# Optimization experiments

Hardware: AMD Instinct MI355X
Metric: run time of the kernel (lower is better)

The kernel has to match this reference:

```python
import jax, jax.numpy as jnp
import numpy as np

D = 1152      # model dim
E = 4         # num_experts
HID = 768     # llama FFN hidden: multiple_of*ceil(int(2*1152/3)/256)
NH = 8        # cross-attention heads
TEMP = 2.0    # expert gumbel temperature (eval: no decay)


def _gumbel_softmax(key, logits, temp, hard):
    g = jax.random.gumbel(key, logits.shape, logits.dtype)
    y = jax.nn.softmax((logits + g) / temp, axis=-1)
    if hard:
        oh = jax.nn.one_hot(jnp.argmax(y, axis=-1), logits.shape[-1], dtype=logits.dtype)
        y = oh - jax.lax.stop_gradient(y) + y
    return y


def _mha(x, mem, in_w, in_b, out_w, out_b):
    # torch nn.MultiheadAttention(batch_first=True): packed qkv in_proj.
    B, S, Dm = x.shape
    hd = Dm // NH
    q = x @ in_w[:Dm].T + in_b[:Dm]
    k = mem @ in_w[Dm:2 * Dm].T + in_b[Dm:2 * Dm]
    v = mem @ in_w[2 * Dm:].T + in_b[2 * Dm:]
    q = q.reshape(B, S, NH, hd).transpose(0, 2, 1, 3)
    k = k.reshape(B, -1, NH, hd).transpose(0, 2, 1, 3)
    v = v.reshape(B, -1, NH, hd).transpose(0, 2, 1, 3)
    a = jax.nn.softmax(jnp.einsum('bhqd,bhkd->bhqk', q, k) / jnp.sqrt(jnp.asarray(hd, x.dtype)), axis=-1)
    o = jnp.einsum('bhqk,bhkd->bhqd', a, v).transpose(0, 2, 1, 3).reshape(B, S, Dm)
    return o @ out_w.T + out_b


def _ff_all(x2d, w1, w2, w3):
    # all E llama SwiGLU experts densely: x2d [N,D], w1/w3 [E,HID,D], w2 [E,D,HID] -> [N,E,D]
    h1 = jnp.einsum('nd,ehd->neh', x2d, w1)
    h3 = jnp.einsum('nd,ehd->neh', x2d, w3)
    return jnp.einsum('neh,edh->ned', jax.nn.silu(h1) * h3, w2)


def setup_inputs() -> dict:
    key = jax.random.key(0)
    ks = jax.random.split(key, 32)
    s = 0.02
    B, S, Sc = 2, 1024, 128
    inp = {
        'x': jax.random.normal(ks[0], (B, S, D), jnp.float32),
        'time': jax.random.normal(ks[1], (B, D), jnp.float32),
        'caption': jax.random.normal(ks[2], (B, Sc, D), jnp.float32),
        'acoustic': jax.random.normal(ks[3], (B, S, D), jnp.float32),
        'attn_in_w': jax.random.normal(ks[4], (3 * D, D), jnp.float32) * s,
        'attn_in_b': jnp.zeros((3 * D,), jnp.float32),
        'attn_out_w': jax.random.normal(ks[5], (D, D), jnp.float32) * s,
        'attn_out_b': jnp.zeros((D,), jnp.float32),
        'hl_w': jax.random.normal(ks[6], (2, D), jnp.float32) * s,
        'hl_b': jnp.zeros((2,), jnp.float32),
        'cap_gate_w': jax.random.normal(ks[7], (E, D), jnp.float32) * s,
        'cap_gate_b': jnp.zeros((E,), jnp.float32),
        'ac_gate_w': jax.random.normal(ks[8], (E, D), jnp.float32) * s,
        'ac_gate_b': jnp.zeros((E,), jnp.float32),
        'cap_w1': jax.random.normal(ks[9], (E, HID, D), jnp.float32) * s,
        'cap_w2': jax.random.normal(ks[10], (E, D, HID), jnp.float32) * s,
        'cap_w3': jax.random.normal(ks[11], (E, HID, D), jnp.float32) * s,
        'ac_w1': jax.random.normal(ks[12], (E, HID, D), jnp.float32) * s,
        'ac_w2': jax.random.normal(ks[13], (E, D, HID), jnp.float32) * s,
        'ac_w3': jax.random.normal(ks[14], (E, HID, D), jnp.float32) * s,
        'fr_w1': jax.random.normal(ks[15], (E, HID, D), jnp.float32) * s,
        'fr_w2': jax.random.normal(ks[16], (E, D, HID), jnp.float32) * s,
        'fr_w3': jax.random.normal(ks[17], (E, HID, D), jnp.float32) * s,
    }
    return inp


def reference(x, time, caption, acoustic,
              attn_in_w, attn_in_b, attn_out_w, attn_out_b,
              hl_w, hl_b, cap_gate_w, cap_gate_b, ac_gate_w, ac_gate_b,
              cap_w1, cap_w2, cap_w3, ac_w1, ac_w2, ac_w3,
              fr_w1, fr_w2, fr_w3):
    B, S, Dm = x.shape
    # cross-attention: x attends over caption, output replaces caption stream
    ca = _mha(x, caption, attn_in_w, attn_in_b, attn_out_w, attn_out_b)
    cap2 = ca.reshape(-1, Dm)          # [N, D]
    x2 = x.reshape(-1, Dm)             # [N, D]
    ac2 = acoustic.reshape(-1, Dm)     # [N, D]
    # high-level caption/acoustic gate from time embedding, broadcast over tokens
    hl = jnp.repeat(time @ hl_w.T + hl_b, S, axis=0)  # [N, 2]
    k1, k2, k3 = jax.random.split(jax.random.key(42), 3)
    hp = _gumbel_softmax(k1, hl, 1.0, False)
    cm = hp[:, 0:1]   # caption mask [N,1]
    am = hp[:, 1:2]   # acoustic mask [N,1]
    # expert gates (eval: hard one-hot straight-through)
    cp = _gumbel_softmax(k2, cap2 @ cap_gate_w.T + cap_gate_b, TEMP, True)  # [N,E]
    ap = _gumbel_softmax(k3, ac2 @ ac_gate_w.T + ac_gate_b, TEMP, True)    # [N,E]
    # dense per-expert SwiGLU, masked combine
    zc = jnp.einsum('ned,ne->nd', _ff_all(x2, cap_w1, cap_w2, cap_w3), cp) * cm
    za = jnp.einsum('ned,ne->nd', _ff_all(x2, ac_w1, ac_w2, ac_w3), ap) * am
    y = (zc + za).reshape(B, S, Dm)
    # frequency experts: each expert sees y masked to its channel block, keeps its block
    r = Dm // E
    region = ((jnp.arange(Dm)[None, :] // r) == jnp.arange(E)[:, None]).astype(x.dtype)  # [E,D]
    ym = y[None] * region[:, None, None, :]  # [E,B,S,D]
    h1 = jnp.einsum('ebsd,ehd->ebsh', ym, fr_w1)
    h3 = jnp.einsum('ebsd,ehd->ebsh', ym, fr_w3)
    fo = jnp.einsum('ebsh,edh->ebsd', jax.nn.silu(h1) * h3, fr_w2)  # [E,B,S,D]
    z = jnp.concatenate([fo[e, :, :, e * r:(e + 1) * r] for e in range(E)], axis=-1)
    # load balancing loss
    probs = jnp.concatenate([cp, ap], axis=1)                                  # [N,2E]
    masks = jnp.concatenate([jnp.tile(cm, (1, E)), jnp.tile(am, (1, E))], axis=1)
    usage = (probs * masks).sum(axis=0) / (masks.sum() + 1e-10)
    lb_loss = jnp.mean(usage * jnp.log(usage + 1e-10))
    return z, lb_loss
```

## Files before the change

kernel.cpp:

```cpp
#include <hip/hip_runtime.h>
#include <stdint.h>

#define NDIM 1152
#define NEXP 4
#define NHID 768
#define NHEAD 8
#define HDIM 144
#define NB 2
#define NS 1024
#define NSC 128
#define NTOK 2048
#define NCAP 256

typedef _Float16 f16;
typedef _Float16 f16x4 __attribute__((ext_vector_type(4)));
typedef _Float16 f16x8 __attribute__((ext_vector_type(8)));
typedef float f32x4 __attribute__((ext_vector_type(4)));

#define MFMA16(a, b, c) __builtin_amdgcn_mfma_f32_16x16x32_f16(a, b, c, 0, 0, 0)

#define WSZ ((size_t)NEXP * NHID * NDIM)
#define WCH ((size_t)(WSZ / 8))

__device__ inline uint2 tfry(uint32_t k0, uint32_t k1, uint32_t x0, uint32_t x1) {
  uint32_t k2 = k0 ^ k1 ^ 0x1BD11BDAu;
#define RND(r) { x0 += x1; x1 = (x1 << r) | (x1 >> (32 - r)); x1 ^= x0; }
  x0 += k0; x1 += k1;
  RND(13) RND(15) RND(26) RND(6)
  x0 += k1; x1 += k2 + 1u;
  RND(17) RND(29) RND(16) RND(24)
  x0 += k2; x1 += k0 + 2u;
  RND(13) RND(15) RND(26) RND(6)
  x0 += k0; x1 += k1 + 3u;
  RND(17) RND(29) RND(16) RND(24)
  x0 += k1; x1 += k2 + 4u;
  RND(13) RND(15) RND(26) RND(6)
  x0 += k2; x1 += k0 + 5u;
#undef RND
  return make_uint2(x0, x1);
}

__device__ inline float b2g(uint32_t bits) {
  uint32_t fb = (bits >> 9) | 0x3f800000u;
  float f = __uint_as_float(fb) - 1.0f;
  const float tiny = 1.1754943508222875e-38f;
  float u = f * 1.0f + tiny;
  u = fmaxf(tiny, u);
  return -logf(-logf(u));
}

__global__ void k_prep(const float* __restrict__ timep, const float* __restrict__ hlw,
                       const float* __restrict__ hlb,
                       float* __restrict__ g1, float* __restrict__ g2, float* __restrict__ g3,
                       float* __restrict__ tl) {
  int t = threadIdx.x;
  uint2 k1 = tfry(0u, 42u, 0u, 0u);
  uint2 k2 = tfry(0u, 42u, 0u, 1u);
  uint2 k3 = tfry(0u, 42u, 0u, 2u);
  for (int p = t; p < 4096; p += 256) {
    uint2 o = tfry(k1.x, k1.y, 0u, (uint32_t)p);
    g1[p] = b2g(o.x ^ o.y);
  }
  for (int p = t; p < 8192; p += 256) {
    uint2 o2 = tfry(k2.x, k2.y, 0u, (uint32_t)p);
    g2[p] = b2g(o2.x ^ o2.y);
    uint2 o3 = tfry(k3.x, k3.y, 0u, (uint32_t)p);
    g3[p] = b2g(o3.x ^ o3.y);
  }
  int wv = t >> 6, lane = t & 63;
  {
    int b = wv >> 1, j = wv & 1;
    float s = 0.f;
    for (int k = lane; k < NDIM; k += 64) s += timep[b * NDIM + k] * hlw[j * NDIM + k];
    for (int m = 32; m; m >>= 1) s += __shfl_xor(s, m);
    if (lane == 0) tl[b * 2 + j] = s + hlb[j];
  }
}

__global__ void k_ac_logits(const float* __restrict__ ac, const float* __restrict__ agw,
                            const float* __restrict__ agb, float* __restrict__ al) {
  int wv = threadIdx.x >> 6, lane = threadIdx.x & 63;
  int n = blockIdx.x * 4 + wv;
  float s[NEXP] = {0.f, 0.f, 0.f, 0.f};
  for (int d = lane; d < NDIM; d += 64) {
    float a = ac[(size_t)n * NDIM + d];
#pragma unroll
    for (int e = 0; e < NEXP; ++e) s[e] += a * agw[e * NDIM + d];
  }
#pragma unroll
  for (int e = 0; e < NEXP; ++e)
    for (int m = 32; m; m >>= 1) s[e] += __shfl_xor(s[e], m);
  if (lane == 0) {
#pragma unroll
    for (int e = 0; e < NEXP; ++e) al[n * NEXP + e] = s[e] + agb[e];
  }
}

__global__ void k_cvt_add(const float* __restrict__ srca, const float* __restrict__ srcb,
                          f16* __restrict__ dst, int n) {
  int i = (blockIdx.x * 256 + threadIdx.x) * 4;
  if (i + 3 < n) {
    float4 va = *(const float4*)(srca + i);
    float4 vb = *(const float4*)(srcb + i);
    f16x4 h;
    h[0] = (f16)(va.x + vb.x); h[1] = (f16)(va.y + vb.y);
    h[2] = (f16)(va.z + vb.z); h[3] = (f16)(va.w + vb.w);
    *(f16x4*)(dst + i) = h;
  }
}

__global__ void k_cvt_split(const float* __restrict__ src, f16* __restrict__ hi,
                            f16* __restrict__ lo, int n) {
  int i = (blockIdx.x * 256 + threadIdx.x) * 4;
  if (i + 3 < n) {
    float4 v = *(const float4*)(src + i);
    f16x4 h, l;
    h[0] = (f16)v.x; l[0] = (f16)((v.x - (float)h[0]) * 2048.f);
    h[1] = (f16)v.y; l[1] = (f16)((v.y - (float)h[1]) * 2048.f);
    h[2] = (f16)v.z; l[2] = (f16)((v.z - (float)h[2]) * 2048.f);
    h[3] = (f16)v.w; l[3] = (f16)((v.w - (float)h[3]) * 2048.f);
    *(f16x4*)(hi + i) = h;
    *(f16x4*)(lo + i) = l;
  }
}

__global__ __launch_bounds__(256) void k_gemm_qkv(
    const f16* __restrict__ xhi, const f16* __restrict__ xlo,
    const f16* __restrict__ caphi, const f16* __restrict__ caplo,
    const float* __restrict__ inw, const float* __restrict__ inb,
    f16* __restrict__ qhi, f16* __restrict__ qlo,
    f16* __restrict__ khi, f16* __restrict__ klo,
    f16* __restrict__ vthi, f16* __restrict__ vtlo,
    const float* __restrict__ w0, const float* __restrict__ w1,
    const float* __restrict__ w2, const float* __restrict__ w3,
    f16* __restrict__ wf16) {
  int z = blockIdx.z;
  if (z >= 3) {
    int cvtid = (z - 3) * 576 + blockIdx.y * 18 + blockIdx.x;
    size_t c0 = (size_t)cvtid * 1536;
    int slot = (int)(c0 / WCH);
    size_t base = (c0 % WCH) * 8;
    const float* s = ((slot == 0) ? w0 : (slot == 1) ? w1 : (slot == 2) ? w2 : w3) + base;
    f16* dst = wf16 + (size_t)slot * WSZ + base;
#pragma unroll
    for (int i = 0; i < 6; ++i) {
      size_t off = (size_t)(threadIdx.x + i * 256) * 8;
      float4 v0 = *(const float4*)(s + off);
      float4 v1 = *(const float4*)(s + off + 4);
      f16x8 h;
      h[0] = (f16)v0.x; h[1] = (f16)v0.y; h[2] = (f16)v0.z; h[3] = (f16)v0.w;
      h[4] = (f16)v1.x; h[5] = (f16)v1.y; h[6] = (f16)v1.z; h[7] = (f16)v1.w;
      *(f16x8*)(dst + off) = h;
    }
    return;
  }
  int M = (z == 0) ? NTOK : NCAP;
  int mt = blockIdx.y, nt = blockIdx.x;
  if (mt * 64 >= M) return;
  const f16* Ah_g = (z == 0) ? xhi : caphi;
  const f16* Al_g = (z == 0) ? xlo : caplo;
  __shared__ f16 Ash[64 * 72];
  __shared__ f16 Asl[64 * 72];
  __shared__ f16 Bsh[64 * 72];
  __shared__ f16 Bsl[64 * 72];
  int t = threadIdx.x;
  int wv = t >> 6, lane = t & 63, m16 = lane & 15, quad = lane >> 4;
  int r0 = t >> 3, ak = (t & 7) * 8;
  size_t a0o = (size_t)(mt * 64 + r0) * NDIM;
  size_t a1o = (size_t)(mt * 64 + r0 + 32) * NDIM;
  f32x4 zf = {0.f, 0.f, 0.f, 0.f};
  f32x4 ah[2][2] = {{zf, zf}, {zf, zf}};
  f32x4 am[2][2] = {{zf, zf}, {zf, zf}};
  uint4 rah0, rah1, ral0, ral1;
  float4 rbw[4];
  rah0 = *(const uint4*)(Ah_g + a0o + ak);
  rah1 = *(const uint4*)(Ah_g + a1o + ak);
  ral0 = *(const uint4*)(Al_g + a0o + ak);
  ral1 = *(const uint4*)(Al_g + a1o + ak);
#pragma unroll
  for (int uu = 0; uu < 4; ++uu) {
    int u = t + uu * 256;
    int rr = u >> 4, kp = (u & 15) * 4;
    rbw[uu] = *(const float4*)(inw + (size_t)(z * NDIM + nt * 64 + rr) * NDIM + kp);
  }
  for (int kc = 0; kc < NDIM; kc += 64) {
    __syncthreads();
    *(uint4*)&Ash[r0 * 72 + ak] = rah0;
    *(uint4*)&Ash[(r0 + 32) * 72 + ak] = rah1;
    *(uint4*)&Asl[r0 * 72 + ak] = ral0;
    *(uint4*)&Asl[(r0 + 32) * 72 + ak] = ral1;
#pragma unroll
    for (int uu = 0; uu < 4; ++uu) {
      int u = t + uu * 256;
      int rr = u >> 4, kp = (u & 15) * 4;
      f16x4 hb, lb;
      hb[0] = (f16)rbw[uu].x; lb[0] = (f16)((rbw[uu].x - (float)hb[0]) * 2048.f);
      hb[1] = (f16)rbw[uu].y; lb[1] = (f16)((rbw[uu].y - (float)hb[1]) * 2048.f);
      hb[2] = (f16)rbw[uu].z; lb[2] = (f16)((rbw[uu].z - (float)hb[2]) * 2048.f);
      hb[3] = (f16)rbw[uu].w; lb[3] = (f16)((rbw[uu].w - (float)hb[3]) * 2048.f);
      *(f16x4*)&Bsh[rr * 72 + kp] = hb;
      *(f16x4*)&Bsl[rr * 72 + kp] = lb;
    }
    __syncthreads();
    int kn = kc + 64;
    if (kn < NDIM) {
      rah0 = *(const uint4*)(Ah_g + a0o + kn + ak);
      rah1 = *(const uint4*)(Ah_g + a1o + kn + ak);
      ral0 = *(const uint4*)(Al_g + a0o + kn + ak);
      ral1 = *(const uint4*)(Al_g + a1o + kn + ak);
#pragma unroll
      for (int uu = 0; uu < 4; ++uu) {
        int u = t + uu * 256;
        int rr = u >> 4, kp = (u & 15) * 4;
        rbw[uu] = *(const float4*)(inw + (size_t)(z * NDIM + nt * 64 + rr) * NDIM + kn + kp);
      }
    }
#pragma unroll
    for (int ks = 0; ks < 2; ++ks) {
      int aoff = ((wv & 1) * 32 + m16) * 72 + ks * 32 + quad * 8;
      int boff = ((wv >> 1) * 32 + m16) * 72 + ks * 32 + quad * 8;
      f16x8 a0h = *(const f16x8*)&Ash[aoff];
      f16x8 a1h = *(const f16x8*)&Ash[aoff + 16 * 72];
      f16x8 a0l = *(const f16x8*)&Asl[aoff];
      f16x8 a1l = *(const f16x8*)&Asl[aoff + 16 * 72];
      f16x8 b0h = *(const f16x8*)&Bsh[boff];
      f16x8 b1h = *(const f16x8*)&Bsh[boff + 16 * 72];
      f16x8 b0l = *(const f16x8*)&Bsl[boff];
      f16x8 b1l = *(const f16x8*)&Bsl[boff + 16 * 72];
      ah[0][0] = MFMA16(a0h, b0h, ah[0][0]);
      ah[0][1] = MFMA16(a0h, b1h, ah[0][1]);
      ah[1][0] = MFMA16(a1h, b0h, ah[1][0]);
      ah[1][1] = MFMA16(a1h, b1h, ah[1][1]);
      am[0][0] = MFMA16(a0h, b0l, am[0][0]);
      am[0][1] = MFMA16(a0h, b1l, am[0][1]);
      am[1][0] = MFMA16(a1h, b0l, am[1][0]);
      am[1][1] = MFMA16(a1h, b1l, am[1][1]);
      am[0][0] = MFMA16(a0l, b0h, am[0][0]);
      am[0][1] = MFMA16(a0l, b1h, am[0][1]);
      am[1][0] = MFMA16(a1l, b0h, am[1][0]);
      am[1][1] = MFMA16(a1l, b1h, am[1][1]);
    }
  }
#pragma unroll
  for (int mi = 0; mi < 2; ++mi)
#pragma unroll
    for (int ni = 0; ni < 2; ++ni)
#pragma unroll
// ... 23 lines not shown
__global__ __launch_bounds__(256) void k_attn(
    const f16* __restrict__ qhi, const f16* __restrict__ qlo,
    const f16* __restrict__ khi, const f16* __restrict__ klo,
    const f16* __restrict__ vthi, const f16* __restrict__ vtlo,
    f16* __restrict__ ohi, f16* __restrict__ olo) {
  int mt = blockIdx.x, bh = blockIdx.y;
  int b = bh >> 3, h = bh & 7;
  __shared__ f16 Ah[64 * 160];
  __shared__ f16 Al[64 * 160];
  __shared__ f16 Bh[32 * 160];
  __shared__ f16 Bl[32 * 160];
  __shared__ f16 Ph[64 * 136];
  __shared__ f16 Pl[64 * 136];
  int t = threadIdx.x;
  int wv = t >> 6, lane = t & 63, m16 = lane & 15, quad = lane >> 4;
  for (int u = t; u < 64 * 20; u += 256) {
    int r = u / 20, kp = (u % 20) * 8;
    uint4 vh = make_uint4(0u, 0u, 0u, 0u), vl = vh;
    if (kp < HDIM) {
      size_t gi = (size_t)(b * NS + mt * 64 + r) * NDIM + h * HDIM + kp;
      vh = *(const uint4*)&qhi[gi];
      vl = *(const uint4*)&qlo[gi];
    }
    *(uint4*)&Ah[r * 160 + kp] = vh;
    *(uint4*)&Al[r * 160 + kp] = vl;
  }
  __syncthreads();
  f16x8 ahf[5], alf[5];
#pragma unroll
  for (int ks = 0; ks < 5; ++ks) {
    int ao = (wv * 16 + m16) * 160 + ks * 32 + quad * 8;
    ahf[ks] = *(const f16x8*)&Ah[ao];
    alf[ks] = *(const f16x8*)&Al[ao];
  }
  f32x4 zf = {0.f, 0.f, 0.f, 0.f};
  f32x4 sh_[4][2], sm_[4][2];
#pragma unroll
  for (int kt = 0; kt < 4; ++kt)
#pragma unroll
    for (int ni = 0; ni < 2; ++ni) { sh_[kt][ni] = zf; sm_[kt][ni] = zf; }
  for (int kt = 0; kt < 4; ++kt) {
    if (kt) __syncthreads();
    for (int u = t; u < 32 * 20; u += 256) {
      int r = u / 20, kp = (u % 20) * 8;
      uint4 vh = make_uint4(0u, 0u, 0u, 0u), vl = vh;
      if (kp < HDIM) {
        size_t gi = (size_t)(b * NSC + kt * 32 + r) * NDIM + h * HDIM + kp;
        vh = *(const uint4*)&khi[gi];
        vl = *(const uint4*)&klo[gi];
      }
      *(uint4*)&Bh[r * 160 + kp] = vh;
      *(uint4*)&Bl[r * 160 + kp] = vl;
    }
    __syncthreads();
#pragma unroll
    for (int ks = 0; ks < 5; ++ks) {
#pragma unroll
      for (int ni = 0; ni < 2; ++ni) {
        int bo = (ni * 16 + m16) * 160 + ks * 32 + quad * 8;
        f16x8 bhf = *(const f16x8*)&Bh[bo];
        f16x8 blf = *(const f16x8*)&Bl[bo];
        sh_[kt][ni] = MFMA16(ahf[ks], bhf, sh_[kt][ni]);
        sm_[kt][ni] = MFMA16(ahf[ks], blf, sm_[kt][ni]);
        sm_[kt][ni] = MFMA16(alf[ks], bhf, sm_[kt][ni]);
      }
    }
  }
  float sv[4][2][4];
  float mx[4] = {-1e30f, -1e30f, -1e30f, -1e30f};
#pragma unroll
  for (int kt = 0; kt < 4; ++kt)
#pragma unroll
    for (int ni = 0; ni < 2; ++ni)
#pragma unroll
      for (int r = 0; r < 4; ++r) {
        float s = (sh_[kt][ni][r] + sm_[kt][ni][r] * (1.f / 2048.f)) * (1.f / 12.f);
        sv[kt][ni][r] = s;
        mx[r] = fmaxf(mx[r], s);
      }
#pragma unroll
  for (int r = 0; r < 4; ++r) {
    mx[r] = fmaxf(mx[r], __shfl_xor(mx[r], 1));
    mx[r] = fmaxf(mx[r], __shfl_xor(mx[r], 2));
    mx[r] = fmaxf(mx[r], __shfl_xor(mx[r], 4));
    mx[r] = fmaxf(mx[r], __shfl_xor(mx[r], 8));
  }
  float sum[4] = {0.f, 0.f, 0.f, 0.f};
#pragma unroll
  for (int kt = 0; kt < 4; ++kt)
#pragma unroll
    for (int ni = 0; ni < 2; ++ni)
#pragma unroll
      for (int r = 0; r < 4; ++r) {
        float e = expf(sv[kt][ni][r] - mx[r]);
        sv[kt][ni][r] = e;
        sum[r] += e;
      }
  float inv[4];
#pragma unroll
  for (int r = 0; r < 4; ++r) {
    sum[r] += __shfl_xor(sum[r], 1);
    sum[r] += __shfl_xor(sum[r], 2);
    sum[r] += __shfl_xor(sum[r], 4);
    sum[r] += __shfl_xor(sum[r], 8);
    inv[r] = 1.0f / sum[r];
  }
#pragma unroll
  for (int kt = 0; kt < 4; ++kt)
#pragma unroll
    for (int ni = 0; ni < 2; ++ni)
#pragma unroll
      for (int r = 0; r < 4; ++r) {
        float p = sv[kt][ni][r] * inv[r];
        int row = wv * 16 + quad * 4 + r;
        int col = kt * 32 + ni * 16 + m16;
        f16 ph = (f16)p;
        Ph[row * 136 + col] = ph;
        Pl[row * 136 + col] = (f16)((p - (float)ph) * 2048.f);
      }
  const f16* vbh = vthi + (size_t)(b * NDIM + h * HDIM) * NSC;
  const f16* vbl = vtlo + (size_t)(b * NDIM + h * HDIM) * NSC;
  f32x4 oh_[9], om_[9];
#pragma unroll
  for (int nb = 0; nb < 9; ++nb) { oh_[nb] = zf; om_[nb] = zf; }
#pragma unroll
  for (int ks = 0; ks < 4; ++ks) {
    int po = (wv * 16 + m16) * 136 + ks * 32 + quad * 8;
    f16x8 pah = *(const f16x8*)&Ph[po];
    f16x8 pal = *(const f16x8*)&Pl[po];
#pragma unroll
    for (int nb = 0; nb < 9; ++nb) {
      size_t vo = (size_t)(nb * 16 + m16) * NSC + ks * 32 + quad * 8;
      f16x8 bvh = *(const f16x8*)&vbh[vo];
      f16x8 bvl = *(const f16x8*)&vbl[vo];
      oh_[nb] = MFMA16(pah, bvh, oh_[nb]);
      om_[nb] = MFMA16(pah, bvl, om_[nb]);
      om_[nb] = MFMA16(pal, bvh, om_[nb]);
    }
  }
#pragma unroll
  for (int nb = 0; nb < 9; ++nb)
#pragma unroll
    for (int r = 0; r < 4; ++r) {
      int row = mt * 64 + wv * 16 + quad * 4 + r;
      int col = h * HDIM + nb * 16 + m16;
      float v = oh_[nb][r] + om_[nb][r] * (1.f / 2048.f);
      size_t idx = (size_t)(b * NS + row) * NDIM + col;
      f16 hv = (f16)v;
      ohi[idx] = hv;
      olo[idx] = (f16)((v - (float)hv) * 2048.f);
    }
}

__global__ __launch_bounds__(256) void k_ca(
    const f16* __restrict__ ohi, const f16* __restrict__ olo,
    const float* __restrict__ ow, const float* __restrict__ ob,
    float* __restrict__ ca,
    const float* __restrict__ w4, const float* __restrict__ w5,
    const float* __restrict__ w6, const float* __restrict__ w7,
    const float* __restrict__ w8, f16* __restrict__ wf16) {
  int z = blockIdx.z;
  if (z >= 1) {
    int cvtid = (z - 1) * 576 + blockIdx.y * 18 + blockIdx.x;
    if (cvtid >= 1080) return;
    size_t c0 = (size_t)cvtid * 2048;
    int sg = (int)(c0 / WCH);
    size_t base = (c0 % WCH) * 8;
    const float* s = ((sg == 0) ? w4 : (sg == 1) ? w5 : (sg == 2) ? w6
                       : (sg == 3) ? w7 : w8) + base;
    f16* dst = wf16 + (size_t)(4 + sg) * WSZ + base;
#pragma unroll
    for (int i = 0; i < 8; ++i) {
      size_t off = (size_t)(threadIdx.x + i * 256) * 8;
      float4 v0 = *(const float4*)(s + off);
      float4 v1 = *(const float4*)(s + off + 4);
      f16x8 h;
      h[0] = (f16)v0.x; h[1] = (f16)v0.y; h[2] = (f16)v0.z; h[3] = (f16)v0.w;
      h[4] = (f16)v1.x; h[5] = (f16)v1.y; h[6] = (f16)v1.z; h[7] = (f16)v1.w;
      *(f16x8*)(dst + off) = h;
    }
    return;
  }
  int mt = blockIdx.y, nt = blockIdx.x;
  __shared__ f16 Ash[64 * 72];
  __shared__ f16 Asl[64 * 72];
  __shared__ f16 Bsh[64 * 72];
  __shared__ f16 Bsl[64 * 72];
  int t = threadIdx.x;
  int wv = t >> 6, lane = t & 63, m16 = lane & 15, quad = lane >> 4;
  int r0 = t >> 3, ak = (t & 7) * 8;
  size_t a0o = (size_t)(mt * 64 + r0) * NDIM;
  size_t a1o = (size_t)(mt * 64 + r0 + 32) * NDIM;
  f32x4 zf = {0.f, 0.f, 0.f, 0.f};
  f32x4 ah[2][2] = {{zf, zf}, {zf, zf}};
  f32x4 am[2][2] = {{zf, zf}, {zf, zf}};
  uint4 rah0, rah1, ral0, ral1;
  float4 rbw[4];
  rah0 = *(const uint4*)(ohi + a0o + ak);
  rah1 = *(const uint4*)(ohi + a1o + ak);
  ral0 = *(const uint4*)(olo + a0o + ak);
  ral1 = *(const uint4*)(olo + a1o + ak);
#pragma unroll
  for (int uu = 0; uu < 4; ++uu) {
    int u = t + uu * 256;
    int rr = u >> 4, kp = (u & 15) * 4;
    rbw[uu] = *(const float4*)(ow + (size_t)(nt * 64 + rr) * NDIM + kp);
  }
  for (int kc = 0; kc < NDIM; kc += 64) {
    __syncthreads();
    *(uint4*)&Ash[r0 * 72 + ak] = rah0;
    *(uint4*)&Ash[(r0 + 32) * 72 + ak] = rah1;
    *(uint4*)&Asl[r0 * 72 + ak] = ral0;
    *(uint4*)&Asl[(r0 + 32) * 72 + ak] = ral1;
#pragma unroll
    for (int uu = 0; uu < 4; ++uu) {
      int u = t + uu * 256;
      int rr = u >> 4, kp = (u & 15) * 4;
      f16x4 hb, lb;
      hb[0] = (f16)rbw[uu].x; lb[0] = (f16)((rbw[uu].x - (float)hb[0]) * 2048.f);
      hb[1] = (f16)rbw[uu].y; lb[1] = (f16)((rbw[uu].y - (float)hb[1]) * 2048.f);
      hb[2] = (f16)rbw[uu].z; lb[2] = (f16)((rbw[uu].z - (float)hb[2]) * 2048.f);
      hb[3] = (f16)rbw[uu].w; lb[3] = (f16)((rbw[uu].w - (float)hb[3]) * 2048.f);
      *(f16x4*)&Bsh[rr * 72 + kp] = hb;
      *(f16x4*)&Bsl[rr * 72 + kp] = lb;
    }
    __syncthreads();
    int kn = kc + 64;
    if (kn < NDIM) {
      rah0 = *(const uint4*)(ohi + a0o + kn + ak);
      rah1 = *(const uint4*)(ohi + a1o + kn + ak);
      ral0 = *(const uint4*)(olo + a0o + kn + ak);
      ral1 = *(const uint4*)(olo + a1o + kn + ak);
#pragma unroll
      for (int uu = 0; uu < 4; ++uu) {
        int u = t + uu * 256;
        int rr = u >> 4, kp = (u & 15) * 4;
        rbw[uu] = *(const float4*)(ow + (size_t)(nt * 64 + rr) * NDIM + kn + kp);
      }
    }
#pragma unroll
    for (int ks = 0; ks < 2; ++ks) {
      int aoff = ((wv & 1) * 32 + m16) * 72 + ks * 32 + quad * 8;
      int boff = ((wv >> 1) * 32 + m16) * 72 + ks * 32 + quad * 8;
      f16x8 a0h = *(const f16x8*)&Ash[aoff];
      f16x8 a1h = *(const f16x8*)&Ash[aoff + 16 * 72];
      f16x8 a0l = *(const f16x8*)&Asl[aoff];
      f16x8 a1l = *(const f16x8*)&Asl[aoff + 16 * 72];
      f16x8 b0h = *(const f16x8*)&Bsh[boff];
      f16x8 b1h = *(const f16x8*)&Bsh[boff + 16 * 72];
      f16x8 b0l = *(const f16x8*)&Bsl[boff];
      f16x8 b1l = *(const f16x8*)&Bsl[boff + 16 * 72];
      ah[0][0] = MFMA16(a0h, b0h, ah[0][0]);
      ah[0][1] = MFMA16(a0h, b1h, ah[0][1]);
      ah[1][0] = MFMA16(a1h, b0h, ah[1][0]);
      ah[1][1] = MFMA16(a1h, b1h, ah[1][1]);
      am[0][0] = MFMA16(a0h, b0l, am[0][0]);
      am[0][1] = MFMA16(a0h, b1l, am[0][1]);
      am[1][0] = MFMA16(a1h, b0l, am[1][0]);
      am[1][1] = MFMA16(a1h, b1l, am[1][1]);
      am[0][0] = MFMA16(a0l, b0h, am[0][0]);
      am[0][1] = MFMA16(a0l, b1h, am[0][1]);
      am[1][0] = MFMA16(a1l, b0h, am[1][0]);
      am[1][1] = MFMA16(a1l, b1h, am[1][1]);
    }
  }
#pragma unroll
  for (int mi = 0; mi < 2; ++mi)
#pragma unroll
    for (int ni = 0; ni < 2; ++ni)
#pragma unroll
      for (int r = 0; r < 4; ++r) {
        int row = mt * 64 + (wv & 1) * 32 + mi * 16 + quad * 4 + r;
        int col = nt * 64 + (wv >> 1) * 32 + ni * 16 + m16;
        ca[(size_t)row * NDIM + col] =
            ah[mi][ni][r] + am[mi][ni][r] * (1.f / 2048.f) + ob[col];
      }
}

__global__ __launch_bounds__(1024) void k_route(
    const float* __restrict__ cl, const float* __restrict__ al,
    const float* __restrict__ g1, const float* __restrict__ g2,
    const float* __restrict__ g3, const float* __restrict__ tl,
    float* __restrict__ cmv, float* __restrict__ amv,
    int* __restrict__ lists, int* __restrict__ counts, float* __restrict__ out_loss) {
  __shared__ int lcnt[8];
  __shared__ float bins[8];
  __shared__ float ssum[2];
  int t = threadIdx.x;
  if (t < 8) { lcnt[t] = 0; bins[t] = 0.f; }
  if (t < 2) ssum[t] = 0.f;
  __syncthreads();
  for (int n = t; n < NTOK; n += 1024) {
    float lc[NEXP];
#pragma unroll
    for (int e = 0; e < NEXP; ++e) lc[e] = cl[n * NEXP + e] + g2[n * 4 + e];
    int ec = 0; float bv = lc[0];
#pragma unroll
    for (int e = 1; e < NEXP; ++e) if (lc[e] > bv) { bv = lc[e]; ec = e; }
    float la[NEXP];
#pragma unroll
    for (int e = 0; e < NEXP; ++e) la[e] = al[n * NEXP + e] + g3[n * 4 + e];
    int ea = 0; float bva = la[0];
#pragma unroll
    for (int e = 1; e < NEXP; ++e) if (la[e] > bva) { bva = la[e]; ea = e; }
    int b = n >> 10;
    float a0 = tl[b * 2 + 0] + g1[n * 2 + 0];
    float a1 = tl[b * 2 + 1] + g1[n * 2 + 1];
    float mx = fmaxf(a0, a1);
    float e0 = expf(a0 - mx), e1 = expf(a1 - mx);
    float cm = e0 / (e0 + e1), am = e1 / (e0 + e1);
    cmv[n] = cm; amv[n] = am;
    int p0 = atomicAdd(&lcnt[ec], 1);
    lists[ec * NTOK + p0] = n;
    int p1 = atomicAdd(&lcnt[4 + ea], 1);
    lists[(4 + ea) * NTOK + p1] = n;
    atomicAdd(&bins[ec], cm);
    atomicAdd(&bins[4 + ea], am);
    atomicAdd(&ssum[0], cm);
    atomicAdd(&ssum[1], am);
  }
  __syncthreads();
  if (t < 8) counts[t] = lcnt[t];
  if (t == 0) {
    float denom = 4.f * (ssum[0] + ssum[1]) + 1e-10f;
    float acc = 0.f;
    for (int j = 0; j < 8; ++j) {
      float u = bins[j] / denom;
      acc += u * logf(u + 1e-10f);
    }
    out_loss[0] = acc / 8.f;
  }
}

__global__ __launch_bounds__(256) void k_gemm1(
    const f16* __restrict__ x16, const f16* __restrict__ y16,
    const f16* __restrict__ wf,
    const int* __restrict__ lists, const int* __restrict__ counts,
    f16* __restrict__ tbuf, int gbase, int G) {
  int bid = blockIdx.x;
  int xcd = bid & 7;
  int local = bid >> 3;
  int ppx = (G * 12) >> 3;
  int pair = xcd * ppx + (local >> 5);
  int mt = local & 31;
  int g = gbase + pair / 12;
  int nt = pair % 12;
  const f16* A; const f16* B1; const f16* B3; f16* tout;
  const int* list = nullptr;
  int cnt, koff, K;
  if (g < 8) {
    int e = g & 3;
    cnt = counts[g];
    list = lists + g * NTOK;
    A = x16; koff = 0; K = NDIM;
    B1 = wf + (size_t)((g < 4) ? 0 : 2) * WSZ + (size_t)e * NHID * NDIM;
    B3 = wf + (size_t)((g < 4) ? 1 : 3) * WSZ + (size_t)e * NHID * NDIM;
    tout = tbuf + (size_t)g * NTOK * NHID;
  } else {
    int e = g - 8;
    cnt = NTOK;
    A = y16; koff = e * 288; K = 288;
    B1 = wf + (size_t)4 * WSZ + (size_t)e * NHID * NDIM + koff;
    B3 = wf + (size_t)5 * WSZ + (size_t)e * NHID * NDIM + koff;
    tout = tbuf + (size_t)e * NTOK * NHID;
  }
  if (mt * 64 >= cnt) return;
  int t = threadIdx.x;
  int wv = t >> 6, lane = t & 63, m16 = lane & 15, quad = lane >> 4;
  int r0 = t >> 3, ak = (t & 7) * 8;
  int m0 = mt * 64 + r0, m1 = m0 + 32;
  int tok0, tok1;
  if (list) { tok0 = list[min(m0, cnt - 1)]; tok1 = list[min(m1, cnt - 1)]; }
  else { tok0 = m0; tok1 = m1; }
  const f16* ar0 = A + (size_t)tok0 * NDIM + koff;
  const f16* ar1 = A + (size_t)tok1 * NDIM + koff;
  const f16* b1r0 = B1 + (size_t)(nt * 64 + r0) * NDIM;
  const f16* b1r1 = B1 + (size_t)(nt * 64 + r0 + 32) * NDIM;
  const f16* b3r0 = B3 + (size_t)(nt * 64 + r0) * NDIM;
  const f16* b3r1 = B3 + (size_t)(nt * 64 + r0 + 32) * NDIM;
  __shared__ f16 As[64 * 72];
  __shared__ f16 Bs1[64 * 72];
  __shared__ f16 Bs2[64 * 72];
  f32x4 zf = {0.f, 0.f, 0.f, 0.f};
  f32x4 ac1[2][2] = {{zf, zf}, {zf, zf}};
  f32x4 ac2[2][2] = {{zf, zf}, {zf, zf}};
  uint4 z4u = make_uint4(0u, 0u, 0u, 0u);
  uint4 ra0, ra1, rb10, rb11, rb30, rb31;
  {
    bool v = (ak < K);
    ra0  = v ? *(const uint4*)(ar0 + ak) : z4u;
    ra1  = v ? *(const uint4*)(ar1 + ak) : z4u;
    rb10 = v ? *(const uint4*)(b1r0 + ak) : z4u;
    rb11 = v ? *(const uint4*)(b1r1 + ak) : z4u;
    rb30 = v ? *(const uint4*)(b3r0 + ak) : z4u;
    rb31 = v ? *(const uint4*)(b3r1 + ak) : z4u;
  }
  for (int kc = 0; kc < K; kc += 64) {
    __syncthreads();
    *(uint4*)&As[r0 * 72 + ak] = ra0;
    *(uint4*)&As[(r0 + 32) * 72 + ak] = ra1;
    *(uint4*)&Bs1[r0 * 72 + ak] = rb10;
    *(uint4*)&Bs1[(r0 + 32) * 72 + ak] = rb11;
    *(uint4*)&Bs2[r0 * 72 + ak] = rb30;
    *(uint4*)&Bs2[(r0 + 32) * 72 + ak] = rb31;
    __syncthreads();
    int kn = kc + 64;
    if (kn < K) {
      bool v = (kn + ak < K);
      ra0  = v ? *(const uint4*)(ar0 + kn + ak) : z4u;
      ra1  = v ? *(const uint4*)(ar1 + kn + ak) : z4u;
      rb10 = v ? *(const uint4*)(b1r0 + kn + ak) : z4u;
      rb11 = v ? *(const uint4*)(b1r1 + kn + ak) : z4u;
      rb30 = v ? *(const uint4*)(b3r0 + kn + ak) : z4u;
      rb31 = v ? *(const uint4*)(b3r1 + kn + ak) : z4u;
    }
#pragma unroll
    for (int ks = 0; ks < 2; ++ks) {
      int aoff = ((wv & 1) * 32 + m16) * 72 + ks * 32 + quad * 8;
      int boff = ((wv >> 1) * 32 + m16) * 72 + ks * 32 + quad * 8;
      f16x8 a0 = *(const f16x8*)&As[aoff];
      f16x8 a1 = *(const f16x8*)&As[aoff + 16 * 72];
      f16x8 b10 = *(const f16x8*)&Bs1[boff];
      f16x8 b11 = *(const f16x8*)&Bs1[boff + 16 * 72];
      f16x8 b30 = *(const f16x8*)&Bs2[boff];
      f16x8 b31 = *(const f16x8*)&Bs2[boff + 16 * 72];
      ac1[0][0] = MFMA16(a0, b10, ac1[0][0]);
      ac1[0][1] = MFMA16(a0, b11, ac1[0][1]);
      ac1[1][0] = MFMA16(a1, b10, ac1[1][0]);
      ac1[1][1] = MFMA16(a1, b11, ac1[1][1]);
      ac2[0][0] = MFMA16(a0, b30, ac2[0][0]);
      ac2[0][1] = MFMA16(a0, b31, ac2[0][1]);
      ac2[1][0] = MFMA16(a1, b30, ac2[1][0]);
      ac2[1][1] = MFMA16(a1, b31, ac2[1][1]);
    }
  }
#pragma unroll
  for (int mi = 0; mi < 2; ++mi)
#pragma unroll
    for (int ni = 0; ni < 2; ++ni)
#pragma unroll
      for (int r = 0; r < 4; ++r) {
        int row = mt * 64 + (wv & 1) * 32 + mi * 16 + quad * 4 + r;
        int col = nt * 64 + (wv >> 1) * 32 + ni * 16 + m16;
        float h1 = ac1[mi][ni][r];
        float h3 = ac2[mi][ni][r];
        float sl = h1 / (1.0f + expf(-h1));
        tout[(size_t)row * NHID + col] = (f16)(sl * h3);
      }
}

__global__ __launch_bounds__(256) void k_gemm2(
    const f16* __restrict__ tbuf, const f16* __restrict__ wf,
    const int* __restrict__ lists, const int* __restrict__ counts,
    const float* __restrict__ cmv, const float* __restrict__ amv,
    float* __restrict__ yc, float* __restrict__ ya) {
  int bid = blockIdx.x;
  int xcd = bid & 7;
  int local = bid >> 3;
  int pair = xcd * 18 + (local >> 5);
  int mt = local & 31;
  int g = pair / 18;
  int nt = pair % 18;
  int e = g & 3;
  int cnt = counts[g];
  if (mt * 64 >= cnt) return;
  const int* list = lists + g * NTOK;
  const f16* A = tbuf + (size_t)g * NTOK * NHID;
  const f16* Bw = wf + (size_t)((g < 4) ? 6 : 7) * WSZ + (size_t)e * NDIM * NHID;
  const float* sc = (g < 4) ? cmv : amv;
  float* y = (g < 4) ? yc : ya;
  int t = threadIdx.x;
  int wv = t >> 6, lane = t & 63, m16 = lane & 15, quad = lane >> 4;
  int r0 = t >> 3, ak = (t & 7) * 8;
  const f16* ar0 = A + (size_t)(mt * 64 + r0) * NHID;
  const f16* ar1 = A + (size_t)(mt * 64 + r0 + 32) * NHID;
  const f16* br0 = Bw + (size_t)(nt * 64 + r0) * NHID;
  const f16* br1 = Bw + (size_t)(nt * 64 + r0 + 32) * NHID;
  __shared__ f16 As[64 * 72];
  __shared__ f16 Bs[64 * 72];
  f32x4 zf = {0.f, 0.f, 0.f, 0.f};
  f32x4 acc[2][2] = {{zf, zf}, {zf, zf}};
  uint4 ra0, ra1, rb0, rb1;
  ra0 = *(const uint4*)(ar0 + ak);
  ra1 = *(const uint4*)(ar1 + ak);
  rb0 = *(const uint4*)(br0 + ak);
  rb1 = *(const uint4*)(br1 + ak);
  for (int kc = 0; kc < NHID; kc += 64) {
    __syncthreads();
    *(uint4*)&As[r0 * 72 + ak] = ra0;
    *(uint4*)&As[(r0 + 32) * 72 + ak] = ra1;
    *(uint4*)&Bs[r0 * 72 + ak] = rb0;
    *(uint4*)&Bs[(r0 + 32) * 72 + ak] = rb1;
    __syncthreads();
    int kn = kc + 64;
    if (kn < NHID) {
      ra0 = *(const uint4*)(ar0 + kn + ak);
      ra1 = *(const uint4*)(ar1 + kn + ak);
      rb0 = *(const uint4*)(br0 + kn + ak);
      rb1 = *(const uint4*)(br1 + kn + ak);
    }
#pragma unroll
    for (int ks = 0; ks < 2; ++ks) {
      int aoff = ((wv & 1) * 32 + m16) * 72 + ks * 32 + quad * 8;
      int boff = ((wv >> 1) * 32 + m16) * 72 + ks * 32 + quad * 8;
      f16x8 a0 = *(const f16x8*)&As[aoff];
      f16x8 a1 = *(const f16x8*)&As[aoff + 16 * 72];
      f16x8 b0 = *(const f16x8*)&Bs[boff];
      f16x8 b1 = *(const f16x8*)&Bs[boff + 16 * 72];
      acc[0][0] = MFMA16(a0, b0, acc[0][0]);
      acc[0][1] = MFMA16(a0, b1, acc[0][1]);
      acc[1][0] = MFMA16(a1, b0, acc[1][0]);
      acc[1][1] = MFMA16(a1, b1, acc[1][1]);
    }
  }
#pragma unroll
  for (int mi = 0; mi < 2; ++mi)
#pragma unroll
    for (int ni = 0; ni < 2; ++ni)
#pragma unroll
      for (int r = 0; r < 4; ++r) {
        int mg = mt * 64 + (wv & 1) * 32 + mi * 16 + quad * 4 + r;
        if (mg < cnt) {
          int tok = list[mg];
          int col = nt * 64 + (wv >> 1) * 32 + ni * 16 + m16;
          float v = acc[mi][ni][r] * sc[tok];
          y[(size_t)tok * NDIM + col] = v;
        }
      }
}

__global__ __launch_bounds__(256) void k_gemm2_fr(
    const f16* __restrict__ tbuf, const f16* __restrict__ wf, float* __restrict__ zz) {
  int e = blockIdx.z;
  int mt = blockIdx.y, nt = blockIdx.x;
  const f16* A = tbuf + (size_t)e * NTOK * NHID;
  const f16* Bw = wf + (size_t)8 * WSZ + (size_t)e * NDIM * NHID;
  int t = threadIdx.x;
  int wv = t >> 6, lane = t & 63, m16 = lane & 15, quad = lane >> 4;
  int r0 = t >> 3, ak = (t & 7) * 8;
  const f16* ar0 = A + (size_t)(mt * 64 + r0) * NHID;
  const f16* ar1 = A + (size_t)(mt * 64 + r0 + 32) * NHID;
  int ne0 = min(nt * 64 + r0, 287), ne1 = min(nt * 64 + r0 + 32, 287);
  const f16* br0 = Bw + (size_t)(e * 288 + ne0) * NHID;
  const f16* br1 = Bw + (size_t)(e * 288 + ne1) * NHID;
  __shared__ f16 As[64 * 72];
  __shared__ f16 Bs[64 * 72];
  f32x4 zf = {0.f, 0.f, 0.f, 0.f};
  f32x4 acc[2][2] = {{zf, zf}, {zf, zf}};
  uint4 ra0, ra1, rb0, rb1;
  ra0 = *(const uint4*)(ar0 + ak);
  ra1 = *(const uint4*)(ar1 + ak);
  rb0 = *(const uint4*)(br0 + ak);
  rb1 = *(const uint4*)(br1 + ak);
  for (int kc = 0; kc < NHID; kc += 64) {
    __syncthreads();
    *(uint4*)&As[r0 * 72 + ak] = ra0;
    *(uint4*)&As[(r0 + 32) * 72 + ak] = ra1;
    *(uint4*)&Bs[r0 * 72 + ak] = rb0;
    *(uint4*)&Bs[(r0 + 32) * 72 + ak] = rb1;
    __syncthreads();
    int kn = kc + 64;
    if (kn < NHID) {
      ra0 = *(const uint4*)(ar0 + kn + ak);
      ra1 = *(const uint4*)(ar1 + kn + ak);
      rb0 = *(const uint4*)(br0 + kn + ak);
      rb1 = *(const uint4*)(br1 + kn + ak);
    }
#pragma unroll
    for (int ks = 0; ks < 2; ++ks) {
      int aoff = ((wv & 1) * 32 + m16) * 72 + ks * 32 + quad * 8;
      int boff = ((wv >> 1) * 32 + m16) * 72 + ks * 32 + quad * 8;
      f16x8 a0 = *(const f16x8*)&As[aoff];
      f16x8 a1 = *(const f16x8*)&As[aoff + 16 * 72];
      f16x8 b0 = *(const f16x8*)&Bs[boff];
      f16x8 b1 = *(const f16x8*)&Bs[boff + 16 * 72];
      acc[0][0] = MFMA16(a0, b0, acc[0][0]);
      acc[0][1] = MFMA16(a0, b1, acc[0][1]);
      acc[1][0] = MFMA16(a1, b0, acc[1][0]);
      acc[1][1] = MFMA16(a1, b1, acc[1][1]);
    }
  }
#pragma unroll
  for (int mi = 0; mi < 2; ++mi)
#pragma unroll
    for (int ni = 0; ni < 2; ++ni)
#pragma unroll
      for (int r = 0; r < 4; ++r) {
        int cg = nt * 64 + (wv >> 1) * 32 + ni * 16 + m16;
        if (cg < 288) {
          int row = mt * 64 + (wv & 1) * 32 + mi * 16 + quad * 4 + r;
          zz[(size_t)row * NDIM + e * 288 + cg] = acc[mi][ni][r];
        }
      }
}

extern "C" void kernel_launch(void* const* d_in, const int* in_sizes, int n_in,
                              void* d_out, int out_size, void* d_ws, size_t ws_size,
                              hipStream_t stream) {
  const float* x          = (const float*)d_in[0];
  const float* timep      = (const float*)d_in[1];
  const float* caption    = (const float*)d_in[2];
  const float* acoustic   = (const float*)d_in[3];
  const float* attn_in_w  = (const float*)d_in[4];
  const float* attn_in_b  = (const float*)d_in[5];
  const float* attn_out_w = (const float*)d_in[6];
  const float* attn_out_b = (const float*)d_in[7];
  const float* hl_w       = (const float*)d_in[8];
  const float* hl_b       = (const float*)d_in[9];
  const float* cap_gate_w = (const float*)d_in[10];
  const float* cap_gate_b = (const float*)d_in[11];
  const float* ac_gate_w  = (const float*)d_in[12];
  const float* ac_gate_b  = (const float*)d_in[13];
  const float* cap_w1     = (const float*)d_in[14];
  const float* cap_w2     = (const float*)d_in[15];
  const float* cap_w3     = (const float*)d_in[16];
  const float* ac_w1      = (const float*)d_in[17];
  const float* ac_w2      = (const float*)d_in[18];
  const float* ac_w3      = (const float*)d_in[19];
  const float* fr_w1      = (const float*)d_in[20];
  const float* fr_w2      = (const float*)d_in[21];
  const float* fr_w3      = (const float*)d_in[22];
  (void)in_sizes; (void)n_in; (void)out_size; (void)ws_size;

  float* zout = (float*)d_out;
  float* loss = zout + (size_t)NTOK * NDIM;

  char* wsb = (char*)d_ws;
  size_t off = 0;
  auto alloc = [&](size_t bytes) -> void* {
    void* p = wsb + off;
    off = (off + bytes + 255) & ~(size_t)255;
    return p;
  };
  float* g1     = (float*)alloc(4096 * 4);
  float* g2     = (float*)alloc(8192 * 4);
  float* g3     = (float*)alloc(8192 * 4);
  float* tl     = (float*)alloc(4 * 4);
  float* al     = (float*)alloc((size_t)NTOK * NEXP * 4);
  float* cl     = (float*)alloc((size_t)NTOK * NEXP * 4);
  float* cmv    = (float*)alloc((size_t)NTOK * 4);
  float* amv    = (float*)alloc((size_t)NTOK * 4);
  int*   lists  = (int*)alloc((size_t)8 * NTOK * 4);
  int*   counts = (int*)alloc(8 * 4);
  f16*   xhi    = (f16*)alloc((size_t)NTOK * NDIM * 2);
  f16*   wf16   = (f16*)alloc((size_t)9 * WSZ * 2);
  size_t region = off;
  f16*   xlo    = (f16*)alloc((size_t)NTOK * NDIM * 2);
  f16*   caphi  = (f16*)alloc((size_t)NCAP * NDIM * 2);
  f16*   caplo  = (f16*)alloc((size_t)NCAP * NDIM * 2);
  f16*   qhi    = (f16*)alloc((size_t)NTOK * NDIM * 2);
  f16*   qlo    = (f16*)alloc((size_t)NTOK * NDIM * 2);
  f16*   khi    = (f16*)alloc((size_t)NCAP * NDIM * 2);
  f16*   klo    = (f16*)alloc((size_t)NCAP * NDIM * 2);
  f16*   vthi   = (f16*)alloc((size_t)NB * NDIM * NSC * 2);
  f16*   vtlo   = (f16*)alloc((size_t)NB * NDIM * NSC * 2);
  f16*   ohi    = (f16*)alloc((size_t)NTOK * NDIM * 2);
  f16*   olo    = (f16*)alloc((size_t)NTOK * NDIM * 2);
  float* ca32   = (float*)alloc((size_t)NTOK * NDIM * 4);
  off = region;
  f16*   tbuf   = (f16*)alloc((size_t)8 * NTOK * NHID * 2);
  float* ybc    = (float*)alloc((size_t)NTOK * NDIM * 4);
  float* yba    = (float*)alloc((size_t)NTOK * NDIM * 4);
  f16*   y16    = (f16*)alloc((size_t)NTOK * NDIM * 2);

  k_prep<<<dim3(1), dim3(256), 0, stream>>>(timep, hl_w, hl_b, g1, g2, g3, tl);
  k_ac_logits<<<dim3(512), dim3(256), 0, stream>>>(acoustic, ac_gate_w, ac_gate_b, al);
  k_cvt_split<<<dim3(2304), dim3(256), 0, stream>>>(x, xhi, xlo, NTOK * NDIM);
  k_cvt_split<<<dim3(288), dim3(256), 0, stream>>>(caption, caphi, caplo, NCAP * NDIM);
  k_gemm_qkv<<<dim3(18, 32, 5), dim3(256), 0, stream>>>(
      xhi, xlo, caphi, caplo, attn_in_w, attn_in_b,
      qhi, qlo, khi, klo, vthi, vtlo,
      cap_w1, cap_w3, ac_w1, ac_w3, wf16);
  k_attn<<<dim3(16, 16), dim3(256), 0, stream>>>(qhi, qlo, khi, klo, vthi, vtlo, ohi, olo);
  k_ca<<<dim3(18, 32, 3), dim3(256), 0, stream>>>(ohi, olo, attn_out_w, attn_out_b, ca32,
                                                  fr_w1, fr_w3, cap_w2, ac_w2, fr_w2, wf16);
  k_ac_logits<<<dim3(512), dim3(256), 0, stream>>>(ca32, cap_gate_w, cap_gate_b, cl);
  k_route<<<dim3(1), dim3(1024), 0, stream>>>(cl, al, g1, g2, g3, tl,
                                              cmv, amv, lists, counts, loss);
  k_gemm1<<<dim3(3072), dim3(256), 0, stream>>>(xhi, y16, wf16, lists, counts, tbuf, 0, 8);
  k_gemm2<<<dim3(4608), dim3(256), 0, stream>>>(tbuf, wf16, lists, counts,
                                                cmv, amv, ybc, yba);
  k_cvt_add<<<dim3(2304), dim3(256), 0, stream>>>(ybc, yba, y16, NTOK * NDIM);
  k_gemm1<<<dim3(1536), dim3(256), 0, stream>>>(xhi, y16, wf16, lists, counts, tbuf, 8, 4);
  k_gemm2_fr<<<dim3(5, 32, 4), dim3(256), 0, stream>>>(tbuf, wf16, zout);
}
```

Before: 478.9 us.

## Fold attention output projection into the caption gate weights and drop the GEMM

```diff
diff --git a/kernel.cpp b/kernel.cpp
--- a/kernel.cpp
+++ b/kernel.cpp
@@ -77,6 +77,35 @@
   }
 }
 
+__global__ void k_fuse_gate(const float* __restrict__ ow, const float* __restrict__ ob,
+                            const float* __restrict__ gw, const float* __restrict__ gb,
+                            float* __restrict__ wp, float* __restrict__ bp) {
+  int t = threadIdx.x;
+  if (blockIdx.x == 5) {
+    int wv = t >> 6, lane = t & 63;
+    float s = 0.f;
+    for (int d = lane; d < NDIM; d += 64) s += ob[d] * gw[wv * NDIM + d];
+    for (int m = 32; m; m >>= 1) s += __shfl_xor(s, m);
+    if (lane == 0) bp[wv] = s + gb[wv];
+    return;
+  }
+  __shared__ float gws[4 * NDIM];
+  for (int i = t; i < 4 * NDIM; i += 256) gws[i] = gw[i];
+  __syncthreads();
+  int k = blockIdx.x * 256 + t;
+  if (k >= NDIM) return;
+  float a0 = 0.f, a1 = 0.f, a2 = 0.f, a3 = 0.f;
+#pragma unroll 4
+  for (int d = 0; d < NDIM; ++d) {
+    float o = ow[(size_t)d * NDIM + k];
+    a0 += gws[d] * o;
+    a1 += gws[NDIM + d] * o;
+    a2 += gws[2 * NDIM + d] * o;
+    a3 += gws[3 * NDIM + d] * o;
+  }
+  wp[k] = a0; wp[NDIM + k] = a1; wp[2 * NDIM + k] = a2; wp[3 * NDIM + k] = a3;
+}
+
 __global__ void k_ac_logits(const float* __restrict__ ac, const float* __restrict__ agw,
                             const float* __restrict__ agb, float* __restrict__ al) {
   int wv = threadIdx.x >> 6, lane = threadIdx.x & 63;
@@ -93,6 +122,27 @@
   if (lane == 0) {
 #pragma unroll
     for (int e = 0; e < NEXP; ++e) al[n * NEXP + e] = s[e] + agb[e];
+  }
+}
+
+__global__ void k_o_logits(const f16* __restrict__ ohi, const f16* __restrict__ olo,
+                           const float* __restrict__ wp, const float* __restrict__ bp,
+                           float* __restrict__ cl) {
+  int wv = threadIdx.x >> 6, lane = threadIdx.x & 63;
+  int n = blockIdx.x * 4 + wv;
+  float s[NEXP] = {0.f, 0.f, 0.f, 0.f};
+  for (int d = lane; d < NDIM; d += 64) {
+    size_t gi = (size_t)n * NDIM + d;
+    float a = (float)ohi[gi] + (float)olo[gi] * (1.f / 2048.f);
+#pragma unroll
+    for (int e = 0; e < NEXP; ++e) s[e] += a * wp[e * NDIM + d];
+  }
+#pragma unroll
+  for (int e = 0; e < NEXP; ++e)
+    for (int m = 32; m; m >>= 1) s[e] += __shfl_xor(s[e], m);
+  if (lane == 0) {
+#pragma unroll
+    for (int e = 0; e < NEXP; ++e) cl[n * NEXP + e] = s[e] + bp[e];
   }
 }
 
@@ -422,131 +472,6 @@
     }
 }
 
-__global__ __launch_bounds__(256) void k_ca(
-    const f16* __restrict__ ohi, const f16* __restrict__ olo,
-    const float* __restrict__ ow, const float* __restrict__ ob,
-    float* __restrict__ ca,
-    const float* __restrict__ w4, const float* __restrict__ w5,
-    const float* __restrict__ w6, const float* __restrict__ w7,
-    const float* __restrict__ w8, f16* __restrict__ wf16) {
-  int z = blockIdx.z;
-  if (z >= 1) {
-    int cvtid = (z - 1) * 576 + blockIdx.y * 18 + blockIdx.x;
-    if (cvtid >= 1080) return;
-    size_t c0 = (size_t)cvtid * 2048;
-    int sg = (int)(c0 / WCH);
-    size_t base = (c0 % WCH) * 8;
-    const float* s = ((sg == 0) ? w4 : (sg == 1) ? w5 : (sg == 2) ? w6
-                       : (sg == 3) ? w7 : w8) + base;
-    f16* dst = wf16 + (size_t)(4 + sg) * WSZ + base;
-#pragma unroll
-    for (int i = 0; i < 8; ++i) {
-      size_t off = (size_t)(threadIdx.x + i * 256) * 8;
-      float4 v0 = *(const float4*)(s + off);
-      float4 v1 = *(const float4*)(s + off + 4);
-      f16x8 h;
-      h[0] = (f16)v0.x; h[1] = (f16)v0.y; h[2] = (f16)v0.z; h[3] = (f16)v0.w;
-      h[4] = (f16)v1.x; h[5] = (f16)v1.y; h[6] = (f16)v1.z; h[7] = (f16)v1.w;
-      *(f16x8*)(dst + off) = h;
-    }
-    return;
-  }
-  int mt = blockIdx.y, nt = blockIdx.x;
-  __shared__ f16 Ash[64 * 72];
-  __shared__ f16 Asl[64 * 72];
-  __shared__ f16 Bsh[64 * 72];
-  __shared__ f16 Bsl[64 * 72];
-  int t = threadIdx.x;
-  int wv = t >> 6, lane = t & 63, m16 = lane & 15, quad = lane >> 4;
-  int r0 = t >> 3, ak = (t & 7) * 8;
-  size_t a0o = (size_t)(mt * 64 + r0) * NDIM;
-  size_t a1o = (size_t)(mt * 64 + r0 + 32) * NDIM;
-  f32x4 zf = {0.f, 0.f, 0.f, 0.f};
-  f32x4 ah[2][2] = {{zf, zf}, {zf, zf}};
-  f32x4 am[2][2] = {{zf, zf}, {zf, zf}};
-  uint4 rah0, rah1, ral0, ral1;
-  float4 rbw[4];
-  rah0 = *(const uint4*)(ohi + a0o + ak);
-  rah1 = *(const uint4*)(ohi + a1o + ak);
-  ral0 = *(const uint4*)(olo + a0o + ak);
-  ral1 = *(const uint4*)(olo + a1o + ak);
-#pragma unroll
-  for (int uu = 0; uu < 4; ++uu) {
-    int u = t + uu * 256;
-    int rr = u >> 4, kp = (u & 15) * 4;
-    rbw[uu] = *(const float4*)(ow + (size_t)(nt * 64 + rr) * NDIM + kp);
-  }
-  for (int kc = 0; kc < NDIM; kc += 64) {
-    __syncthreads();
-    *(uint4*)&Ash[r0 * 72 + ak] = rah0;
-    *(uint4*)&Ash[(r0 + 32) * 72 + ak] = rah1;
-    *(uint4*)&Asl[r0 * 72 + ak] = ral0;
-    *(uint4*)&Asl[(r0 + 32) * 72 + ak] = ral1;
-#pragma unroll
-    for (int uu = 0; uu < 4; ++uu) {
-      int u = t + uu * 256;
-      int rr = u >> 4, kp = (u & 15) * 4;
-      f16x4 hb, lb;
-      hb[0] = (f16)rbw[uu].x; lb[0] = (f16)((rbw[uu].x - (float)hb[0]) * 2048.f);
-      hb[1] = (f16)rbw[uu].y; lb[1] = (f16)((rbw[uu].y - (float)hb[1]) * 2048.f);
-      hb[2] = (f16)rbw[uu].z; lb[2] = (f16)((rbw[uu].z - (float)hb[2]) * 2048.f);
-      hb[3] = (f16)rbw[uu].w; lb[3] = (f16)((rbw[uu].w - (float)hb[3]) * 2048.f);
-      *(f16x4*)&Bsh[rr * 72 + kp] = hb;
-      *(f16x4*)&Bsl[rr * 72 + kp] = lb;
-    }
-    __syncthreads();
-    int kn = kc + 64;
-    if (kn < NDIM) {
-      rah0 = *(const uint4*)(ohi + a0o + kn + ak);
-      rah1 = *(const uint4*)(ohi + a1o + kn + ak);
-      ral0 = *(const uint4*)(olo + a0o + kn + ak);
-      ral1 = *(const uint4*)(olo + a1o + kn + ak);
-#pragma unroll
-      for (int uu = 0; uu < 4; ++uu) {
-        int u = t + uu * 256;
-        int rr = u >> 4, kp = (u & 15) * 4;
-        rbw[uu] = *(const float4*)(ow + (size_t)(nt * 64 + rr) * NDIM + kn + kp);
-      }
-    }
-#pragma unroll
-    for (int ks = 0; ks < 2; ++ks) {
-      int aoff = ((wv & 1) * 32 + m16) * 72 + ks * 32 + quad * 8;
-      int boff = ((wv >> 1) * 32 + m16) * 72 + ks * 32 + quad * 8;
-      f16x8 a0h = *(const f16x8*)&Ash[aoff];
-      f16x8 a1h = *(const f16x8*)&Ash[aoff + 16 * 72];
-      f16x8 a0l = *(const f16x8*)&Asl[aoff];
-      f16x8 a1l = *(const f16x8*)&Asl[aoff + 16 * 72];
-      f16x8 b0h = *(const f16x8*)&Bsh[boff];
-      f16x8 b1h = *(const f16x8*)&Bsh[boff + 16 * 72];
-      f16x8 b0l = *(const f16x8*)&Bsl[boff];
-      f16x8 b1l = *(const f16x8*)&Bsl[boff + 16 * 72];
-      ah[0][0] = MFMA16(a0h, b0h, ah[0][0]);
-      ah[0][1] = MFMA16(a0h, b1h, ah[0][1]);
-      ah[1][0] = MFMA16(a1h, b0h, ah[1][0]);
-      ah[1][1] = MFMA16(a1h, b1h, ah[1][1]);
-      am[0][0] = MFMA16(a0h, b0l, am[0][0]);
-      am[0][1] = MFMA16(a0h, b1l, am[0][1]);
-      am[1][0] = MFMA16(a1h, b0l, am[1][0]);
-      am[1][1] = MFMA16(a1h, b1l, am[1][1]);
-      am[0][0] = MFMA16(a0l, b0h, am[0][0]);
-      am[0][1] = MFMA16(a0l, b1h, am[0][1]);
-      am[1][0] = MFMA16(a1l, b0h, am[1][0]);
-      am[1][1] = MFMA16(a1l, b1h, am[1][1]);
-    }
-  }
-#pragma unroll
-  for (int mi = 0; mi < 2; ++mi)
-#pragma unroll
-    for (int ni = 0; ni < 2; ++ni)
-#pragma unroll
-      for (int r = 0; r < 4; ++r) {
-        int row = mt * 64 + (wv & 1) * 32 + mi * 16 + quad * 4 + r;
-        int col = nt * 64 + (wv >> 1) * 32 + ni * 16 + m16;
-        ca[(size_t)row * NDIM + col] =
-            ah[mi][ni][r] + am[mi][ni][r] * (1.f / 2048.f) + ob[col];
-      }
-}
-
 __global__ __launch_bounds__(1024) void k_route(
     const float* __restrict__ cl, const float* __restrict__ al,
     const float* __restrict__ g1, const float* __restrict__ g2,
@@ -604,10 +529,34 @@
 
 __global__ __launch_bounds__(256) void k_gemm1(
     const f16* __restrict__ x16, const f16* __restrict__ y16,
-    const f16* __restrict__ wf,
+    f16* wf,
     const int* __restrict__ lists, const int* __restrict__ counts,
-    f16* __restrict__ tbuf, int gbase, int G) {
+    f16* __restrict__ tbuf,
+    const float* __restrict__ w4, const float* __restrict__ w5,
+    const float* __restrict__ w6, const float* __restrict__ w7,
+    const float* __restrict__ w8, int gbase, int G) {
   int bid = blockIdx.x;
+  int nblk = G * 384;
+  if (bid >= nblk) {
+    int cvtid = bid - nblk;
+    size_t c0 = (size_t)cvtid * 2048;
+    int sg = (int)(c0 / WCH);
+    size_t base = (c0 % WCH) * 8;
+    const float* s = ((sg == 0) ? w4 : (sg == 1) ? w5 : (sg == 2) ? w6
+                       : (sg == 3) ? w7 : w8) + base;
+    f16* dst = wf + (size_t)(4 + sg) * WSZ + base;
+#pragma unroll
+    for (int i = 0; i < 8; ++i) {
+      size_t off = (size_t)(threadIdx.x + i * 256) * 8;
+      float4 v0 = *(const float4*)(s + off);
+      float4 v1 = *(const float4*)(s + off + 4);
+      f16x8 h;
+      h[0] = (f16)v0.x; h[1] = (f16)v0.y; h[2] = (f16)v0.z; h[3] = (f16)v0.w;
+      h[4] = (f16)v1.x; h[5] = (f16)v1.y; h[6] = (f16)v1.z; h[7] = (f16)v1.w;
+      *(f16x8*)(dst + off) = h;
+    }
+    return;
+  }
   int xcd = bid & 7;
   int local = bid >> 3;
   int ppx = (G * 12) >> 3;
@@ -912,6 +861,8 @@
   float* amv    = (float*)alloc((size_t)NTOK * 4);
   int*   lists  = (int*)alloc((size_t)8 * NTOK * 4);
   int*   counts = (int*)alloc(8 * 4);
+  float* wp     = (float*)alloc((size_t)NEXP * NDIM * 4);
+  float* bp     = (float*)alloc(NEXP * 4);
   f16*   xhi    = (f16*)alloc((size_t)NTOK * NDIM * 2);
   f16*   wf16   = (f16*)alloc((size_t)9 * WSZ * 2);
   size_t region = off;
@@ -926,7 +877,6 @@
   f16*   vtlo   = (f16*)alloc((size_t)NB * NDIM * NSC * 2);
   f16*   ohi    = (f16*)alloc((size_t)NTOK * NDIM * 2);
   f16*   olo    = (f16*)alloc((size_t)NTOK * NDIM * 2);
-  float* ca32   = (float*)alloc((size_t)NTOK * NDIM * 4);
   off = region;
   f16*   tbuf   = (f16*)alloc((size_t)8 * NTOK * NHID * 2);
   float* ybc    = (float*)alloc((size_t)NTOK * NDIM * 4);
@@ -934,6 +884,8 @@
   f16*   y16    = (f16*)alloc((size_t)NTOK * NDIM * 2);
 
   k_prep<<<dim3(1), dim3(256), 0, stream>>>(timep, hl_w, hl_b, g1, g2, g3, tl);
+  k_fuse_gate<<<dim3(6), dim3(256), 0, stream>>>(attn_out_w, attn_out_b,
+                                                 cap_gate_w, cap_gate_b, wp, bp);
   k_ac_logits<<<dim3(512), dim3(256), 0, stream>>>(acoustic, ac_gate_w, ac_gate_b, al);
   k_cvt_split<<<dim3(2304), dim3(256), 0, stream>>>(x, xhi, xlo, NTOK * NDIM);
   k_cvt_split<<<dim3(288), dim3(256), 0, stream>>>(caption, caphi, caplo, NCAP * NDIM);
@@ -942,15 +894,15 @@
       qhi, qlo, khi, klo, vthi, vtlo,
       cap_w1, cap_w3, ac_w1, ac_w3, wf16);
   k_attn<<<dim3(16, 16), dim3(256), 0, stream>>>(qhi, qlo, khi, klo, vthi, vtlo, ohi, olo);
-  k_ca<<<dim3(18, 32, 3), dim3(256), 0, stream>>>(ohi, olo, attn_out_w, attn_out_b, ca32,
-                                                  fr_w1, fr_w3, cap_w2, ac_w2, fr_w2, wf16);
-  k_ac_logits<<<dim3(512), dim3(256), 0, stream>>>(ca32, cap_gate_w, cap_gate_b, cl);
+  k_o_logits<<<dim3(512), dim3(256), 0, stream>>>(ohi, olo, wp, bp, cl);
   k_route<<<dim3(1), dim3(1024), 0, stream>>>(cl, al, g1, g2, g3, tl,
                                               cmv, amv, lists, counts, loss);
-  k_gemm1<<<dim3(3072), dim3(256), 0, stream>>>(xhi, y16, wf16, lists, counts, tbuf, 0, 8);
+  k_gemm1<<<dim3(4152), dim3(256), 0, stream>>>(xhi, y16, wf16, lists, counts, tbuf,
+                                                fr_w1, fr_w3, cap_w2, ac_w2, fr_w2, 0, 8);
   k_gemm2<<<dim3(4608), dim3(256), 0, stream>>>(tbuf, wf16, lists, counts,
                                                 cmv, amv, ybc, yba);
   k_cvt_add<<<dim3(2304), dim3(256), 0, stream>>>(ybc, yba, y16, NTOK * NDIM);
-  k_gemm1<<<dim3(1536), dim3(256), 0, stream>>>(xhi, y16, wf16, lists, counts, tbuf, 8, 4);
+  k_gemm1<<<dim3(1536), dim3(256), 0, stream>>>(xhi, y16, wf16, lists, counts, tbuf,
+                                                fr_w1, fr_w3, cap_w2, ac_w2, fr_w2, 8, 4);
   k_gemm2_fr<<<dim3(5, 32, 4), dim3(256), 0, stream>>>(tbuf, wf16, zout);
 }
```

After: 582.0 us. 21.5% more time.
